# Kernel optimization log

Hardware: AMD Instinct MI355X
Metric: run time of the kernel (lower is better)

Reference implementation:

```python
import jax, jax.numpy as jnp
import numpy as np

H = 1024  # hidden_dim

def setup_inputs() -> dict:
    key = jax.random.key(0)
    ks = jax.random.split(key, 6)
    B, T, D = 4096, 28, 28
    x = jax.random.normal(ks[0], (B, T, D), dtype=jnp.float32)
    key_seq = jax.random.normal(ks[1], (8, T, D), dtype=jnp.float32)
    s_ih = 1.0 / np.sqrt(D)
    s_hh = 1.0 / np.sqrt(H)
    W_ih = jax.random.normal(ks[2], (D, 4 * H), dtype=jnp.float32) * s_ih
    W_hh = jax.random.normal(ks[3], (H, 4 * H), dtype=jnp.float32) * s_hh
    b = jnp.zeros((4 * H,), dtype=jnp.float32)
    W_cls = jax.random.normal(ks[4], (H, 10), dtype=jnp.float32) * s_hh
    b_cls = jnp.zeros((10,), dtype=jnp.float32)
    return {"x": x, "key_seq": key_seq, "W_ih": W_ih, "W_hh": W_hh,
            "b": b, "W_cls": W_cls, "b_cls": b_cls}


def _lstm_last(xs, h0, c0, W_ih, W_hh, b):
    """Run LSTM over xs [B,T,D]; return final (h, c), each [B,H]."""
    xs_t = jnp.swapaxes(xs, 0, 1)  # [T,B,D]

    def step(carry, xt):
        h, c = carry
        g = xt @ W_ih + h @ W_hh + b  # [B,4H]
        i, f, gg, o = jnp.split(g, 4, axis=-1)
        c = jax.nn.sigmoid(f) * c + jax.nn.sigmoid(i) * jnp.tanh(gg)
        h = jax.nn.sigmoid(o) * jnp.tanh(c)
        return (h, c), None

    (h, c), _ = jax.lax.scan(step, (h0, c0), xs_t)
    return h, c


def reference(x, key_seq, W_ih, W_hh, b, W_cls, b_cls):
    B = x.shape[0]
    Kb = key_seq.shape[0]
    zk = jnp.zeros((Kb, H), dtype=x.dtype)
    # key modulation: run the key sequences through the same recurrence;
    # the mean final state seeds the initial state for the data pass.
    hk, ck = _lstm_last(key_seq, zk, zk, W_ih, W_hh, b)
    h0 = jnp.broadcast_to(hk.mean(axis=0), (B, H))
    c0 = jnp.broadcast_to(ck.mean(axis=0), (B, H))
    h, _ = _lstm_last(x, h0, c0, W_ih, W_hh, b)
    # dropout is identity in eval mode
    return h @ W_cls + b_cls  # [B,10]
```

## Files before the change

### kernel.cpp

```cpp
#include <hip/hip_runtime.h>
#include <hip/hip_bf16.h>
#include <stdint.h>

#define HID 1024
#define G4H 4096
#define BATCH 4096
#define TSTEPS 28
#define DIN 28
#define KTOT 1056
#define NKEY 8

typedef __attribute__((ext_vector_type(8))) __bf16 b16x8;
typedef __attribute__((ext_vector_type(4))) __bf16 b16x4;
typedef __attribute__((ext_vector_type(4))) float f32x4;
typedef __attribute__((address_space(1))) unsigned int u32_g;
typedef __attribute__((address_space(3))) unsigned int u32_l;

__device__ __forceinline__ void async16(const __hip_bfloat16* g, __hip_bfloat16* l) {
  __builtin_amdgcn_global_load_lds((u32_g*)g, (u32_l*)l, 16, 0, 0);
}

__device__ __forceinline__ float sigmoidf_(float x) { return 1.f / (1.f + __expf(-x)); }
__device__ __forceinline__ float tanhfast_(float x) { return 2.f / (1.f + __expf(-2.f * x)) - 1.f; }

__global__ __launch_bounds__(256) void prep_weights(
    const float* __restrict__ W_hh, const float* __restrict__ W_ih,
    __hip_bfloat16* __restrict__ Wt, float* __restrict__ kstate) {
  __shared__ float tile[64][65];
  const int k0 = blockIdx.x * 64, n0 = blockIdx.y * 64;
  const int tid = threadIdx.x;
  const int fid = (blockIdx.y * gridDim.x + blockIdx.x) * 256 + tid;
  if (fid < 2 * NKEY * HID) kstate[fid] = 0.f;
  for (int i = tid; i < 4096; i += 256) {
    int kk = i >> 6, nn = i & 63;
    int k = k0 + kk;
    float v = 0.f;
    if (k < HID) v = W_hh[k * G4H + n0 + nn];
    else if (k < HID + DIN) v = W_ih[(k - HID) * G4H + n0 + nn];
    tile[kk][nn] = v;
  }
  __syncthreads();
  for (int i = tid; i < 4096; i += 256) {
    int nn = i >> 6, kk = i & 63;
    int k = k0 + kk;
    if (k < KTOT) Wt[(size_t)(n0 + nn) * KTOT + k] = __float2bfloat16(tile[kk][nn]);
  }
}

__global__ __launch_bounds__(256) void key_step(
    const __hip_bfloat16* __restrict__ Wt, const float* __restrict__ key_seq,
    const float* __restrict__ bias, const float* __restrict__ hk_in,
    float* __restrict__ hk_out, float* __restrict__ ck, int t) {
  __shared__ float sh[NKEY][KTOT];
  __shared__ float sred[32][8][8];
  const int tid = threadIdx.x;
#pragma unroll
  for (int key = 0; key < NKEY; ++key)
    for (int k = tid; k < HID; k += 256) sh[key][k] = hk_in[key * HID + k];
  for (int i = tid; i < NKEY * 32; i += 256) {
    int key = i >> 5, d = i & 31;
    sh[key][HID + d] = (d < DIN) ? key_seq[key * (TSTEPS * DIN) + t * DIN + d] : 0.f;
  }
  __syncthreads();
  const int rowIdx = tid >> 3;
  const int kpart = tid & 7;
  const int gate = rowIdx >> 3, jj = rowIdx & 7;
  const int j0 = blockIdx.x * 8;
  const int n = gate * HID + j0 + jj;
  const __hip_bfloat16* wrow = Wt + (size_t)n * KTOT + kpart * 132;
  const int kb = kpart * 132;
  float acc[NKEY];
#pragma unroll
  for (int key = 0; key < NKEY; ++key) acc[key] = 0.f;
  for (int kk = 0; kk < 132; kk += 4) {
    b16x4 wv = *(const b16x4*)(wrow + kk);
    float w0 = (float)wv[0], w1 = (float)wv[1], w2 = (float)wv[2], w3 = (float)wv[3];
#pragma unroll
    for (int key = 0; key < NKEY; ++key) {
      const float* s = &sh[key][kb + kk];
      acc[key] += w0 * s[0] + w1 * s[1] + w2 * s[2] + w3 * s[3];
    }
  }
#pragma unroll
  for (int key = 0; key < NKEY; ++key) sred[rowIdx][kpart][key] = acc[key];
  __syncthreads();
  if (tid < 64) {
    int key = tid >> 3, j2 = tid & 7;
    float g[4];
#pragma unroll
    for (int gg = 0; gg < 4; ++gg) {
      float s = 0.f;
#pragma unroll
      for (int p = 0; p < 8; ++p) s += sred[gg * 8 + j2][p][key];
      g[gg] = s + bias[gg * HID + j0 + j2];
    }
    size_t ci = (size_t)key * HID + j0 + j2;
    float cv = sigmoidf_(g[1]) * ck[ci] + sigmoidf_(g[0]) * tanhfast_(g[2]);
    ck[ci] = cv;
    hk_out[ci] = sigmoidf_(g[3]) * tanhfast_(cv);
  }
}

__global__ __launch_bounds__(256) void key_mean(
    const float* __restrict__ hk, const float* __restrict__ ck,
    float* __restrict__ h0, float* __restrict__ c0) {
  int j = blockIdx.x * 256 + threadIdx.x;
  float sh_ = 0.f, sc_ = 0.f;
#pragma unroll
  for (int k = 0; k < NKEY; ++k) { sh_ += hk[k * HID + j]; sc_ += ck[k * HID + j]; }
  h0[j] = sh_ * (1.f / NKEY);
  c0[j] = sc_ * (1.f / NKEY);
}

__global__ __launch_bounds__(256) void main_init(
    const float* __restrict__ h0, const float* __restrict__ c0,
    const float* __restrict__ x, __hip_bfloat16* __restrict__ A0,
    __hip_bfloat16* __restrict__ A1, float* __restrict__ c) {
  int idx = blockIdx.x * 256 + threadIdx.x;
  int b = idx / KTOT, col = idx - b * KTOT;
  if (col < HID) {
    A0[idx] = __float2bfloat16(h0[col]);
    c[b * HID + col] = c0[col];
  } else if (col < HID + DIN) {
    A0[idx] = __float2bfloat16(x[b * (TSTEPS * DIN) + (col - HID)]);
  } else {
    A0[idx] = __float2bfloat16(0.f);
    A1[idx] = __float2bfloat16(0.f);
  }
}

__global__ __launch_bounds__(256, 2) void gemm_lstm(
    const __hip_bfloat16* __restrict__ Ain, const __hip_bfloat16* __restrict__ Wt,
    const float* __restrict__ bias, float* __restrict__ cst,
    __hip_bfloat16* __restrict__ Aout, const float* __restrict__ x,
    float* __restrict__ hfin, int t) {
  __shared__ alignas(16) __hip_bfloat16 sA[2][128 * 32];
  __shared__ alignas(16) __hip_bfloat16 sB[2][4 * 32 * 32];
  const int tid = threadIdx.x;
  const int lane = tid & 63, wave = tid >> 6;
  const int wr = wave >> 1, wc = wave & 1;
  const int jt = blockIdx.x, mt = blockIdx.y;
  const int brow = mt * 128, j0 = jt * 32;
  const int lrow = lane & 15, kq = lane >> 4;

  const int kqs = (tid & 3) ^ ((tid >> 3) & 3);
  const int sArow = tid >> 2;
  const int sBstrip = tid >> 7;
  const int sBrow = (tid >> 2) & 31;
  const __hip_bfloat16* gA0 = Ain + (size_t)(brow + sArow) * KTOT + kqs * 8;
  const __hip_bfloat16* gA1 = gA0 + (size_t)64 * KTOT;
  const __hip_bfloat16* gB0 = Wt + (size_t)(sBstrip * HID + j0 + sBrow) * KTOT + kqs * 8;
  const __hip_bfloat16* gB1 = gB0 + (size_t)2 * HID * KTOT;

  int iA[4];
#pragma unroll
  for (int m = 0; m < 4; ++m) {
    int u = (wr * 64 + m * 16 + lrow) * 4 + kq;
    iA[m] = u ^ ((u >> 3) & 3);
  }
  int uB = (wc * 16 + lrow) * 4 + kq;
  const int iB = uB ^ ((uB >> 3) & 3);

  f32x4 acc[4][4] = {};

  async16(gA0, &sA[0][tid * 8]);
  async16(gA1, &sA[0][2048 + tid * 8]);
  async16(gB0, &sB[0][tid * 8]);
  async16(gB1, &sB[0][2048 + tid * 8]);
  __syncthreads();

  for (int it = 0; it < 33; ++it) {
    if (it < 32) {
      const int kt = (it + 1) * 32;
      const int nb = (it + 1) & 1;
      async16(gA0 + kt, &sA[nb][tid * 8]);
      async16(gA1 + kt, &sA[nb][2048 + tid * 8]);
      async16(gB0 + kt, &sB[nb][tid * 8]);
      async16(gB1 + kt, &sB[nb][2048 + tid * 8]);
    }
    const b16x8* sAv = (const b16x8*)sA[it & 1];
    const b16x8* sBv = (const b16x8*)sB[it & 1];
    b16x8 af[4];
#pragma unroll
    for (int m = 0; m < 4; ++m) af[m] = sAv[iA[m]];
    __builtin_amdgcn_s_setprio(1);
#pragma unroll
    for (int g = 0; g < 4; ++g) {
      b16x8 bfr = sBv[g * 128 + iB];
#pragma unroll
      for (int m = 0; m < 4; ++m)
        acc[g][m] = __builtin_amdgcn_mfma_f32_16x16x32_bf16(af[m], bfr, acc[g][m], 0, 0, 0);
    }
    __builtin_amdgcn_s_setprio(0);
    __syncthreads();
  }

  const int jcol = j0 + wc * 16 + lrow;
  const float b_i = bias[jcol], b_f = bias[HID + jcol];
  const float b_g = bias[2 * HID + jcol], b_o = bias[3 * HID + jcol];
#pragma unroll
  for (int m = 0; m < 4; ++m) {
    const int row0 = brow + wr * 64 + m * 16 + (lane >> 4) * 4;
#pragma unroll
    for (int r = 0; r < 4; ++r) {
      const int row = row0 + r;
      const size_t ci = (size_t)row * HID + jcol;
      float gi = acc[0][m][r] + b_i;
      float gf = acc[1][m][r] + b_f;
      float gg = acc[2][m][r] + b_g;
      float go = acc[3][m][r] + b_o;
      float cv = sigmoidf_(gf) * cst[ci] + sigmoidf_(gi) * tanhfast_(gg);
      cst[ci] = cv;
      float h = sigmoidf_(go) * tanhfast_(cv);
      Aout[(size_t)row * KTOT + jcol] = __float2bfloat16(h);
      if (t == TSTEPS - 1) hfin[ci] = h;
    }
  }
  if (jt == 0 && t + 1 < TSTEPS) {
    for (int i = tid; i < 128 * DIN; i += 256) {
      int rr = i / DIN, d = i - rr * DIN;
      Aout[(size_t)(brow + rr) * KTOT + HID + d] =
          __float2bfloat16(x[(size_t)(brow + rr) * (TSTEPS * DIN) + (t + 1) * DIN + d]);
    }
  }
}

__global__ __launch_bounds__(256) void classifier(
    const float* __restrict__ hfin, const float* __restrict__ W_cls,
    const float* __restrict__ b_cls, float* __restrict__ out) {
  __shared__ float sw[HID * 10];
  __shared__ float sred[10][257];
  const int b = blockIdx.x, tid = threadIdx.x;
  for (int i = tid; i < HID * 10; i += 256) sw[i] = W_cls[i];
  __syncthreads();
  float acc[10];
#pragma unroll
  for (int cls = 0; cls < 10; ++cls) acc[cls] = 0.f;
  for (int j = tid; j < HID; j += 256) {
    float hv = hfin[(size_t)b * HID + j];
#pragma unroll
    for (int cls = 0; cls < 10; ++cls) acc[cls] += hv * sw[j * 10 + cls];
  }
#pragma unroll
  for (int cls = 0; cls < 10; ++cls) sred[cls][tid] = acc[cls];
  __syncthreads();
  for (int off = 128; off > 0; off >>= 1) {
    if (tid < off)
#pragma unroll
      for (int cls = 0; cls < 10; ++cls) sred[cls][tid] += sred[cls][tid + off];
    __syncthreads();
  }
  if (tid < 10) out[b * 10 + tid] = sred[tid][0] + b_cls[tid];
}

extern "C" void kernel_launch(void* const* d_in, const int* in_sizes, int n_in,
                              void* d_out, int out_size, void* d_ws, size_t ws_size,
                              hipStream_t stream) {
  const float* x      = (const float*)d_in[0];
  const float* keyseq = (const float*)d_in[1];
  const float* W_ih   = (const float*)d_in[2];
  const float* W_hh   = (const float*)d_in[3];
  const float* bias   = (const float*)d_in[4];
  const float* W_cls  = (const float*)d_in[5];
  const float* b_cls  = (const float*)d_in[6];
  float* out = (float*)d_out;
  (void)in_sizes; (void)n_in; (void)out_size; (void)ws_size;

  char* p = (char*)d_ws;
  auto alloc = [&](size_t bytes) { char* r = p; p += (bytes + 255) & ~(size_t)255; return r; };
  __hip_bfloat16* Wt = (__hip_bfloat16*)alloc((size_t)G4H * KTOT * 2);
  __hip_bfloat16* A0 = (__hip_bfloat16*)alloc((size_t)BATCH * KTOT * 2);
  __hip_bfloat16* A1 = (__hip_bfloat16*)alloc((size_t)BATCH * KTOT * 2);
  float* c    = (float*)alloc((size_t)BATCH * HID * 4);
  float* hfin = (float*)alloc((size_t)BATCH * HID * 4);
  float* hk0  = (float*)alloc((size_t)NKEY * HID * 4);
  float* ck   = (float*)alloc((size_t)NKEY * HID * 4);
  float* hk1  = (float*)alloc((size_t)NKEY * HID * 4);
  float* h0   = (float*)alloc((size_t)HID * 4);
  float* c0   = (float*)alloc((size_t)HID * 4);

  prep_weights<<<dim3(17, 64), 256, 0, stream>>>(W_hh, W_ih, Wt, hk0);

  float* kbuf[2] = {hk0, hk1};
  for (int t = 0; t < TSTEPS; ++t)
    key_step<<<128, 256, 0, stream>>>(Wt, keyseq, bias, kbuf[t & 1], kbuf[(t + 1) & 1], ck, t);
  key_mean<<<4, 256, 0, stream>>>(hk0, ck, h0, c0);

  main_init<<<(BATCH * KTOT) / 256, 256, 0, stream>>>(h0, c0, x, A0, A1, c);

  __hip_bfloat16* Ab[2] = {A0, A1};
  for (int t = 0; t < TSTEPS; ++t)
    gemm_lstm<<<dim3(32, 32), 256, 0, stream>>>(Ab[t & 1], Wt, bias, c,
                                                Ab[(t + 1) & 1], x, hfin, t);
  classifier<<<BATCH, 256, 0, stream>>>(hfin, W_cls, b_cls, out);
}
```

Before: 2.108 ms.

## Enlarge LSTM GEMM tiles to 256x256 with gate-interleaved weight layout

Weights are reordered so the four gates for each 16-column group sit next to each other, which lets a block cover a contiguous 256-row slice of the gate matrix. The recurrent GEMM moves from 128x128 tiles on 256 threads to 256x256 tiles on 512 threads, with a 4-stage LDS ring, split A/B staging and explicit vmcnt waits and barriers. Each wave now does 8x4 MFMA accumulators, raising arithmetic intensity per global load. In exchange there are far fewer blocks (256 per step), one block per CU, more LDS and registers, and a grid that may underfill the GPU.

```diff
diff --git a/kernel.cpp b/kernel.cpp
--- a/kernel.cpp
+++ b/kernel.cpp
@@ -9,6 +9,7 @@
 #define DIN 28
 #define KTOT 1056
 #define NKEY 8
+#define NTILES 33
 
 typedef __attribute__((ext_vector_type(8))) __bf16 b16x8;
 typedef __attribute__((ext_vector_type(4))) __bf16 b16x4;
@@ -22,6 +23,10 @@
 
 __device__ __forceinline__ float sigmoidf_(float x) { return 1.f / (1.f + __expf(-x)); }
 __device__ __forceinline__ float tanhfast_(float x) { return 2.f / (1.f + __expf(-2.f * x)) - 1.f; }
+
+__device__ __forceinline__ int nprime(int gate, int j) {
+  return ((j >> 4) << 6) + (gate << 4) + (j & 15);
+}
 
 __global__ __launch_bounds__(256) void prep_weights(
     const float* __restrict__ W_hh, const float* __restrict__ W_ih,
@@ -43,7 +48,9 @@
   for (int i = tid; i < 4096; i += 256) {
     int nn = i >> 6, kk = i & 63;
     int k = k0 + kk;
-    if (k < KTOT) Wt[(size_t)(n0 + nn) * KTOT + k] = __float2bfloat16(tile[kk][nn]);
+    int n = n0 + nn;
+    int np = nprime(n >> 10, n & 1023);
+    if (k < KTOT) Wt[(size_t)np * KTOT + k] = __float2bfloat16(tile[kk][nn]);
   }
 }
 
@@ -66,8 +73,8 @@
   const int kpart = tid & 7;
   const int gate = rowIdx >> 3, jj = rowIdx & 7;
   const int j0 = blockIdx.x * 8;
-  const int n = gate * HID + j0 + jj;
-  const __hip_bfloat16* wrow = Wt + (size_t)n * KTOT + kpart * 132;
+  const int np = nprime(gate, j0 + jj);
+  const __hip_bfloat16* wrow = Wt + (size_t)np * KTOT + kpart * 132;
   const int kb = kpart * 132;
   float acc[NKEY];
 #pragma unroll
@@ -129,98 +136,109 @@
   }
 }
 
-__global__ __launch_bounds__(256, 2) void gemm_lstm(
+__global__ __launch_bounds__(512, 1) void gemm_lstm(
     const __hip_bfloat16* __restrict__ Ain, const __hip_bfloat16* __restrict__ Wt,
     const float* __restrict__ bias, float* __restrict__ cst,
     __hip_bfloat16* __restrict__ Aout, const float* __restrict__ x,
-    float* __restrict__ hfin, int t) {
-  __shared__ alignas(16) __hip_bfloat16 sA[2][128 * 32];
-  __shared__ alignas(16) __hip_bfloat16 sB[2][4 * 32 * 32];
+    float* __restrict__ hfin, int tstep) {
+  __shared__ alignas(16) __hip_bfloat16 sA[4][256 * 32];
+  __shared__ alignas(16) __hip_bfloat16 sB[4][256 * 32];
   const int tid = threadIdx.x;
   const int lane = tid & 63, wave = tid >> 6;
-  const int wr = wave >> 1, wc = wave & 1;
+  const int wr = wave >> 2, wc = wave & 3;
   const int jt = blockIdx.x, mt = blockIdx.y;
-  const int brow = mt * 128, j0 = jt * 32;
+  const int brow = mt * 256;
   const int lrow = lane & 15, kq = lane >> 4;
-
-  const int kqs = (tid & 3) ^ ((tid >> 3) & 3);
-  const int sArow = tid >> 2;
-  const int sBstrip = tid >> 7;
-  const int sBrow = (tid >> 2) & 31;
-  const __hip_bfloat16* gA0 = Ain + (size_t)(brow + sArow) * KTOT + kqs * 8;
-  const __hip_bfloat16* gA1 = gA0 + (size_t)64 * KTOT;
-  const __hip_bfloat16* gB0 = Wt + (size_t)(sBstrip * HID + j0 + sBrow) * KTOT + kqs * 8;
-  const __hip_bfloat16* gB1 = gB0 + (size_t)2 * HID * KTOT;
-
-  int iA[4];
-#pragma unroll
-  for (int m = 0; m < 4; ++m) {
-    int u = (wr * 64 + m * 16 + lrow) * 4 + kq;
-    iA[m] = u ^ ((u >> 3) & 3);
-  }
-  int uB = (wc * 16 + lrow) * 4 + kq;
-  const int iB = uB ^ ((uB >> 3) & 3);
-
-  f32x4 acc[4][4] = {};
-
-  async16(gA0, &sA[0][tid * 8]);
-  async16(gA1, &sA[0][2048 + tid * 8]);
-  async16(gB0, &sB[0][tid * 8]);
-  async16(gB1, &sB[0][2048 + tid * 8]);
-  __syncthreads();
-
-  for (int it = 0; it < 33; ++it) {
-    if (it < 32) {
-      const int kt = (it + 1) * 32;
-      const int nb = (it + 1) & 1;
-      async16(gA0 + kt, &sA[nb][tid * 8]);
-      async16(gA1 + kt, &sA[nb][2048 + tid * 8]);
-      async16(gB0 + kt, &sB[nb][tid * 8]);
-      async16(gB1 + kt, &sB[nb][2048 + tid * 8]);
-    }
-    const b16x8* sAv = (const b16x8*)sA[it & 1];
-    const b16x8* sBv = (const b16x8*)sB[it & 1];
-    b16x8 af[4];
-#pragma unroll
-    for (int m = 0; m < 4; ++m) af[m] = sAv[iA[m]];
+  const int sx = (lrow >> 1) & 3;
+
+  const int strow = tid >> 2;
+  const int sslot = (tid & 3) ^ ((tid >> 3) & 3);
+  const __hip_bfloat16* gA = Ain + (size_t)(brow + strow) * KTOT + sslot * 8;
+  const __hip_bfloat16* gB = Wt + (size_t)(jt * 256 + strow) * KTOT + sslot * 8;
+  const size_t rstep = (size_t)128 * KTOT;
+
+  int iA[8], iB[4];
+#pragma unroll
+  for (int m = 0; m < 8; ++m) iA[m] = (wr * 128 + m * 16 + lrow) * 4 + (kq ^ sx);
+#pragma unroll
+  for (int g = 0; g < 4; ++g) iB[g] = (wc * 64 + g * 16 + lrow) * 4 + (kq ^ sx);
+
+  f32x4 acc[8][4] = {};
+
+#define STAGE(base, dst, kt) do { \
+    async16((base) + (size_t)(kt) * 32, (dst) + tid * 8); \
+    async16((base) + rstep + (size_t)(kt) * 32, (dst) + 4096 + tid * 8); \
+  } while (0)
+
+  STAGE(gA, sA[0], 0); STAGE(gB, sB[0], 0);
+  STAGE(gA, sA[1], 1); STAGE(gB, sB[1], 1);
+  asm volatile("s_waitcnt vmcnt(4)" ::: "memory");
+  __builtin_amdgcn_s_barrier();
+
+#pragma unroll 1
+  for (int t = 0; t < NTILES; ++t) {
+    const b16x8* cA = (const b16x8*)sA[t & 3];
+    const b16x8* cB = (const b16x8*)sB[t & 3];
+    __hip_bfloat16* pA = sA[(t + 2) & 3];
+    __hip_bfloat16* pB = sB[(t + 2) & 3];
+    b16x8 af[4], bf[4];
+    if (t < NTILES - 2) STAGE(gA, pA, t + 2);
+#pragma unroll
+    for (int m = 0; m < 4; ++m) af[m] = cA[iA[m]];
+#pragma unroll
+    for (int g = 0; g < 4; ++g) bf[g] = cB[iB[g]];
+    __builtin_amdgcn_s_barrier();
     __builtin_amdgcn_s_setprio(1);
 #pragma unroll
-    for (int g = 0; g < 4; ++g) {
-      b16x8 bfr = sBv[g * 128 + iB];
+    for (int g = 0; g < 4; ++g)
 #pragma unroll
       for (int m = 0; m < 4; ++m)
-        acc[g][m] = __builtin_amdgcn_mfma_f32_16x16x32_bf16(af[m], bfr, acc[g][m], 0, 0, 0);
-    }
+        acc[m][g] = __builtin_amdgcn_mfma_f32_16x16x32_bf16(af[m], bf[g], acc[m][g], 0, 0, 0);
     __builtin_amdgcn_s_setprio(0);
-    __syncthreads();
-  }
-
-  const int jcol = j0 + wc * 16 + lrow;
-  const float b_i = bias[jcol], b_f = bias[HID + jcol];
-  const float b_g = bias[2 * HID + jcol], b_o = bias[3 * HID + jcol];
-#pragma unroll
-  for (int m = 0; m < 4; ++m) {
-    const int row0 = brow + wr * 64 + m * 16 + (lane >> 4) * 4;
+    __builtin_amdgcn_s_barrier();
+    if (t < NTILES - 2) STAGE(gB, pB, t + 2);
+#pragma unroll
+    for (int m = 0; m < 4; ++m) af[m] = cA[iA[m + 4]];
+    if (t < NTILES - 2) asm volatile("s_waitcnt vmcnt(4)" ::: "memory");
+    else if (t == NTILES - 2) asm volatile("s_waitcnt vmcnt(0)" ::: "memory");
+    __builtin_amdgcn_s_barrier();
+    __builtin_amdgcn_s_setprio(1);
+#pragma unroll
+    for (int g = 0; g < 4; ++g)
+#pragma unroll
+      for (int m = 0; m < 4; ++m)
+        acc[m + 4][g] = __builtin_amdgcn_mfma_f32_16x16x32_bf16(af[m], bf[g], acc[m + 4][g], 0, 0, 0);
+    __builtin_amdgcn_s_setprio(0);
+    __builtin_amdgcn_s_barrier();
+  }
+#undef STAGE
+
+  const int j = jt * 64 + wc * 16 + lrow;
+  const float b_i = bias[j], b_f = bias[HID + j];
+  const float b_g = bias[2 * HID + j], b_o = bias[3 * HID + j];
+#pragma unroll
+  for (int m = 0; m < 8; ++m) {
+    const int row0 = brow + wr * 128 + m * 16 + kq * 4;
 #pragma unroll
     for (int r = 0; r < 4; ++r) {
       const int row = row0 + r;
-      const size_t ci = (size_t)row * HID + jcol;
-      float gi = acc[0][m][r] + b_i;
-      float gf = acc[1][m][r] + b_f;
-      float gg = acc[2][m][r] + b_g;
-      float go = acc[3][m][r] + b_o;
+      const size_t ci = (size_t)row * HID + j;
+      float gi = acc[m][0][r] + b_i;
+      float gf = acc[m][1][r] + b_f;
+      float gg = acc[m][2][r] + b_g;
+      float go = acc[m][3][r] + b_o;
       float cv = sigmoidf_(gf) * cst[ci] + sigmoidf_(gi) * tanhfast_(gg);
       cst[ci] = cv;
       float h = sigmoidf_(go) * tanhfast_(cv);
-      Aout[(size_t)row * KTOT + jcol] = __float2bfloat16(h);
-      if (t == TSTEPS - 1) hfin[ci] = h;
+      Aout[(size_t)row * KTOT + j] = __float2bfloat16(h);
+      if (tstep == TSTEPS - 1) hfin[ci] = h;
     }
   }
-  if (jt == 0 && t + 1 < TSTEPS) {
-    for (int i = tid; i < 128 * DIN; i += 256) {
+  if (jt == 0 && tstep + 1 < TSTEPS) {
+    for (int i = tid; i < 256 * DIN; i += 512) {
       int rr = i / DIN, d = i - rr * DIN;
       Aout[(size_t)(brow + rr) * KTOT + HID + d] =
-          __float2bfloat16(x[(size_t)(brow + rr) * (TSTEPS * DIN) + (t + 1) * DIN + d]);
+          __float2bfloat16(x[(size_t)(brow + rr) * (TSTEPS * DIN) + (tstep + 1) * DIN + d]);
     }
   }
 }
@@ -290,7 +308,7 @@
 
   __hip_bfloat16* Ab[2] = {A0, A1};
   for (int t = 0; t < TSTEPS; ++t)
-    gemm_lstm<<<dim3(32, 32), 256, 0, stream>>>(Ab[t & 1], Wt, bias, c,
+    gemm_lstm<<<dim3(16, 16), 512, 0, stream>>>(Ab[t & 1], Wt, bias, c,
                                                 Ab[(t + 1) & 1], x, hfin, t);
   classifier<<<BATCH, 256, 0, stream>>>(hfin, W_cls, b_cls, out);
 }
```

Measured after the change: 2.288 ms. +8.5%, slower.

## Deepen GEMM pipeline to four LDS stages and interleave gate rows in weights

Applied to the files above, without the earlier changes.

Replaces the double-buffered K loop with a 4-buffer, 3-tiles-ahead async LDS prefetch. It uses explicit vmcnt waits and raw barriers in place of a full syncthreads each iteration, so global loads can overlap more MFMA work. The transposed weight matrix is also reordered so that the four gate rows for each 16-column group sit next to each other, which makes B-tile loads more contiguous. The LDS swizzle is simplified to match. LDS use per block doubles, which may limit occupancy at two blocks per CU, and the hand-written waitcnt logic risks subtle ordering errors.

```diff
diff --git a/kernel.cpp b/kernel.cpp
--- a/kernel.cpp
+++ b/kernel.cpp
@@ -9,6 +9,7 @@
 #define DIN 28
 #define KTOT 1056
 #define NKEY 8
+#define NTILES 33
 
 typedef __attribute__((ext_vector_type(8))) __bf16 b16x8;
 typedef __attribute__((ext_vector_type(4))) __bf16 b16x4;
@@ -22,6 +23,10 @@
 
 __device__ __forceinline__ float sigmoidf_(float x) { return 1.f / (1.f + __expf(-x)); }
 __device__ __forceinline__ float tanhfast_(float x) { return 2.f / (1.f + __expf(-2.f * x)) - 1.f; }
+
+__device__ __forceinline__ int nprime(int gate, int j) {
+  return ((j >> 4) << 6) + (gate << 4) + (j & 15);
+}
 
 __global__ __launch_bounds__(256) void prep_weights(
     const float* __restrict__ W_hh, const float* __restrict__ W_ih,
@@ -43,7 +48,9 @@
   for (int i = tid; i < 4096; i += 256) {
     int nn = i >> 6, kk = i & 63;
     int k = k0 + kk;
-    if (k < KTOT) Wt[(size_t)(n0 + nn) * KTOT + k] = __float2bfloat16(tile[kk][nn]);
+    int n = n0 + nn;
+    int np = nprime(n >> 10, n & 1023);
+    if (k < KTOT) Wt[(size_t)np * KTOT + k] = __float2bfloat16(tile[kk][nn]);
   }
 }
 
@@ -66,8 +73,8 @@
   const int kpart = tid & 7;
   const int gate = rowIdx >> 3, jj = rowIdx & 7;
   const int j0 = blockIdx.x * 8;
-  const int n = gate * HID + j0 + jj;
-  const __hip_bfloat16* wrow = Wt + (size_t)n * KTOT + kpart * 132;
+  const int np = nprime(gate, j0 + jj);
+  const __hip_bfloat16* wrow = Wt + (size_t)np * KTOT + kpart * 132;
   const int kb = kpart * 132;
   float acc[NKEY];
 #pragma unroll
@@ -134,14 +141,15 @@
     const float* __restrict__ bias, float* __restrict__ cst,
     __hip_bfloat16* __restrict__ Aout, const float* __restrict__ x,
     float* __restrict__ hfin, int t) {
-  __shared__ alignas(16) __hip_bfloat16 sA[2][128 * 32];
-  __shared__ alignas(16) __hip_bfloat16 sB[2][4 * 32 * 32];
+  __shared__ alignas(16) __hip_bfloat16 sA[4][128 * 32];
+  __shared__ alignas(16) __hip_bfloat16 sB[4][4 * 32 * 32];
   const int tid = threadIdx.x;
   const int lane = tid & 63, wave = tid >> 6;
   const int wr = wave >> 1, wc = wave & 1;
   const int jt = blockIdx.x, mt = blockIdx.y;
   const int brow = mt * 128, j0 = jt * 32;
   const int lrow = lane & 15, kq = lane >> 4;
+  const int sx = (lrow >> 1) & 3;
 
   const int kqs = (tid & 3) ^ ((tid >> 3) & 3);
   const int sArow = tid >> 2;
@@ -149,62 +157,68 @@
   const int sBrow = (tid >> 2) & 31;
   const __hip_bfloat16* gA0 = Ain + (size_t)(brow + sArow) * KTOT + kqs * 8;
   const __hip_bfloat16* gA1 = gA0 + (size_t)64 * KTOT;
-  const __hip_bfloat16* gB0 = Wt + (size_t)(sBstrip * HID + j0 + sBrow) * KTOT + kqs * 8;
-  const __hip_bfloat16* gB1 = gB0 + (size_t)2 * HID * KTOT;
+  const __hip_bfloat16* gB0 = Wt + (size_t)nprime(sBstrip, j0 + sBrow) * KTOT + kqs * 8;
+  const __hip_bfloat16* gB1 = Wt + (size_t)nprime(sBstrip + 2, j0 + sBrow) * KTOT + kqs * 8;
 
   int iA[4];
 #pragma unroll
   for (int m = 0; m < 4; ++m) {
-    int u = (wr * 64 + m * 16 + lrow) * 4 + kq;
-    iA[m] = u ^ ((u >> 3) & 3);
-  }
-  int uB = (wc * 16 + lrow) * 4 + kq;
-  const int iB = uB ^ ((uB >> 3) & 3);
+    int row = wr * 64 + m * 16 + lrow;
+    iA[m] = row * 4 + (kq ^ sx);
+  }
+  int iB[4];
+  {
+    int jl = wc * 16 + lrow;
+#pragma unroll
+    for (int g = 0; g < 4; ++g) iB[g] = (g * 32 + jl) * 4 + (kq ^ sx);
+  }
 
   f32x4 acc[4][4] = {};
 
-  async16(gA0, &sA[0][tid * 8]);
-  async16(gA1, &sA[0][2048 + tid * 8]);
-  async16(gB0, &sB[0][tid * 8]);
-  async16(gB1, &sB[0][2048 + tid * 8]);
-  __syncthreads();
-
-  for (int it = 0; it < 33; ++it) {
-    if (it < 32) {
-      const int kt = (it + 1) * 32;
-      const int nb = (it + 1) & 1;
-      async16(gA0 + kt, &sA[nb][tid * 8]);
-      async16(gA1 + kt, &sA[nb][2048 + tid * 8]);
-      async16(gB0 + kt, &sB[nb][tid * 8]);
-      async16(gB1 + kt, &sB[nb][2048 + tid * 8]);
-    }
-    const b16x8* sAv = (const b16x8*)sA[it & 1];
-    const b16x8* sBv = (const b16x8*)sB[it & 1];
-    b16x8 af[4];
-#pragma unroll
-    for (int m = 0; m < 4; ++m) af[m] = sAv[iA[m]];
+#define STAGE(buf, kt) do { \
+    async16(gA0 + (size_t)(kt) * 32, &sA[buf][tid * 8]); \
+    async16(gA1 + (size_t)(kt) * 32, &sA[buf][2048 + tid * 8]); \
+    async16(gB0 + (size_t)(kt) * 32, &sB[buf][tid * 8]); \
+    async16(gB1 + (size_t)(kt) * 32, &sB[buf][2048 + tid * 8]); \
+  } while (0)
+
+  STAGE(0, 0); STAGE(1, 1); STAGE(2, 2);
+  asm volatile("s_waitcnt vmcnt(8)" ::: "memory");
+  __builtin_amdgcn_s_barrier();
+
+  for (int kt = 0; kt < NTILES; ++kt) {
+    if (kt + 3 < NTILES) STAGE((kt + 3) & 3, kt + 3);
+    const b16x8* cA = (const b16x8*)sA[kt & 3];
+    const b16x8* cB = (const b16x8*)sB[kt & 3];
+    b16x8 af[4], bf[4];
+#pragma unroll
+    for (int m = 0; m < 4; ++m) af[m] = cA[iA[m]];
+#pragma unroll
+    for (int g = 0; g < 4; ++g) bf[g] = cB[iB[g]];
     __builtin_amdgcn_s_setprio(1);
 #pragma unroll
-    for (int g = 0; g < 4; ++g) {
-      b16x8 bfr = sBv[g * 128 + iB];
+    for (int g = 0; g < 4; ++g)
 #pragma unroll
       for (int m = 0; m < 4; ++m)
-        acc[g][m] = __builtin_amdgcn_mfma_f32_16x16x32_bf16(af[m], bfr, acc[g][m], 0, 0, 0);
-    }
+        acc[g][m] = __builtin_amdgcn_mfma_f32_16x16x32_bf16(af[m], bf[g], acc[g][m], 0, 0, 0);
     __builtin_amdgcn_s_setprio(0);
-    __syncthreads();
-  }
-
-  const int jcol = j0 + wc * 16 + lrow;
-  const float b_i = bias[jcol], b_f = bias[HID + jcol];
-  const float b_g = bias[2 * HID + jcol], b_o = bias[3 * HID + jcol];
+    if (kt + 3 < NTILES)      asm volatile("s_waitcnt vmcnt(8)" ::: "memory");
+    else if (kt + 2 < NTILES) asm volatile("s_waitcnt vmcnt(4)" ::: "memory");
+    else if (kt + 1 < NTILES) asm volatile("s_waitcnt vmcnt(0)" ::: "memory");
+    __builtin_amdgcn_s_barrier();
+  }
+#undef STAGE
+
+  const int j = j0 + wc * 16 + lrow;
+  const float b_i = bias[j], b_f = bias[HID + j];
+  const float b_g = bias[2 * HID + j], b_o = bias[3 * HID + j];
 #pragma unroll
   for (int m = 0; m < 4; ++m) {
-    const int row0 = brow + wr * 64 + m * 16 + (lane >> 4) * 4;
+    const int row0 = brow + wr * 64 + m * 16 + kq * 4;
 #pragma unroll
     for (int r = 0; r < 4; ++r) {
       const int row = row0 + r;
-      const size_t ci = (size_t)row * HID + jcol;
+      const size_t ci = (size_t)row * HID + j;
       float gi = acc[0][m][r] + b_i;
       float gf = acc[1][m][r] + b_f;
       float gg = acc[2][m][r] + b_g;
@@ -212,7 +226,7 @@
       float cv = sigmoidf_(gf) * cst[ci] + sigmoidf_(gi) * tanhfast_(gg);
       cst[ci] = cv;
       float h = sigmoidf_(go) * tanhfast_(cv);
-      Aout[(size_t)row * KTOT + jcol] = __float2bfloat16(h);
+      Aout[(size_t)row * KTOT + j] = __float2bfloat16(h);
       if (t == TSTEPS - 1) hfin[ci] = h;
     }
   }
```

After: 2.630 ms. 24.8% more time.
